# Kernel optimization log

Measured on AMD Instinct MI355X. Metric: run time of the kernel, lower is better.

Reference implementation:

```python
import jax, jax.numpy as jnp
import numpy as np

T = 1.0  # temperature from __init__


def setup_inputs() -> dict:
    key = jax.random.key(0)
    k1, k2, k3, k4, k5 = jax.random.split(key, 5)
    N, C, NC = 128, 2048, 50000
    Kp, Kn = 4, 508
    inputs = jax.random.normal(k1, (N, C), dtype=jnp.float32)
    positive_index = jax.random.randint(k2, (N, Kp), 0, NC, dtype=jnp.int64)
    negative_index = jax.random.randint(k3, (N, Kn), 0, NC, dtype=jnp.int64)
    cof = jax.random.uniform(k4, (Kp,), dtype=jnp.float32)
    # memory bank buffer (registered buffer M); L2-normalized rows like after updates
    M = jax.random.normal(k5, (NC, C), dtype=jnp.float32)
    M = M / jnp.linalg.norm(M, axis=1, keepdims=True)
    return {"inputs": inputs, "positive_index": positive_index,
            "negative_index": negative_index, "cof": cof, "M": M}


def reference(inputs, positive_index, negative_index, cof, M):
    # index_list: [N, K] with K = Kp + Kn
    index_list = jnp.concatenate([positive_index, negative_index], axis=1)
    # fused gather + batched matmul: logits[n, k] = inputs[n] . M[index_list[n, k]]
    Mg = M[index_list]                                   # [N, K, C] gather
    logits = jnp.einsum('nc,nkc->nk', inputs, Mg) * T    # [N, K]
    # the Python loop over j reuses identical logits; only the CE target column varies
    logp = jax.nn.log_softmax(logits, axis=1)            # [N, K]
    Kp = positive_index.shape[1]
    # loss = sum_j cof[j] * cross_entropy(logits, target=j) = -sum_j cof[j]*mean_n logp[n, j]
    loss = -jnp.sum(cof * jnp.mean(logp[:, :Kp], axis=0))
    return loss, logits
```

## Files before the change

### kernel.cpp

```cpp
#include <hip/hip_runtime.h>

constexpr int N  = 128;
constexpr int C  = 2048;
constexpr int KP = 4;
constexpr int KN = 508;
constexpr int K  = 512;

__global__ __launch_bounds__(256) void logits_kernel(
    const float* __restrict__ inputs,
    const int*   __restrict__ pos_idx,
    const int*   __restrict__ neg_idx,
    const float* __restrict__ M,
    float*       __restrict__ logits)
{
    const int wave = threadIdx.x >> 6;
    const int lane = threadIdx.x & 63;
    const int n    = blockIdx.y;
    const int k    = (blockIdx.x << 2) + wave;

    const int idx = (k < KP) ? pos_idx[n * KP + k]
                             : neg_idx[n * KN + (k - KP)];

    const float4* __restrict__ a = reinterpret_cast<const float4*>(inputs + (size_t)n * C);
    const float4* __restrict__ b = reinterpret_cast<const float4*>(M + (size_t)idx * C);

    float acc = 0.f;
    #pragma unroll
    for (int i = 0; i < C / (4 * 64); ++i) {
        float4 av = a[i * 64 + lane];
        float4 bv = b[i * 64 + lane];
        acc = fmaf(av.x, bv.x, acc);
        acc = fmaf(av.y, bv.y, acc);
        acc = fmaf(av.z, bv.z, acc);
        acc = fmaf(av.w, bv.w, acc);
    }

    #pragma unroll
    for (int off = 32; off > 0; off >>= 1)
        acc += __shfl_down(acc, off, 64);

    if (lane == 0) logits[n * K + k] = acc;
}

__global__ __launch_bounds__(512) void softmax_loss_kernel(
    const float* __restrict__ logits,
    const float* __restrict__ cof,
    float*       __restrict__ row_loss)
{
    __shared__ float red[8];
    __shared__ float xs[KP];
    const int n    = blockIdx.x;
    const int t    = threadIdx.x;
    const int wid  = t >> 6;
    const int lane = t & 63;

    float x = logits[n * K + t];

    float m = x;
    #pragma unroll
    for (int off = 1; off < 64; off <<= 1)
        m = fmaxf(m, __shfl_xor(m, off, 64));
    if (lane == 0) red[wid] = m;
    __syncthreads();
    float bm = red[0];
    #pragma unroll
    for (int i = 1; i < 8; ++i) bm = fmaxf(bm, red[i]);

    float s = expf(x - bm);
    #pragma unroll
    for (int off = 1; off < 64; off <<= 1)
        s += __shfl_xor(s, off, 64);
    __syncthreads();
    if (lane == 0) red[wid] = s;
    if (t < KP) xs[t] = x;
    __syncthreads();

    if (t == 0) {
        float bs = 0.f;
        #pragma unroll
        for (int i = 0; i < 8; ++i) bs += red[i];
        const float logZ = bm + logf(bs);
        float acc = 0.f;
        #pragma unroll
        for (int j = 0; j < KP; ++j)
            acc += cof[j] * (xs[j] - logZ);
        row_loss[n] = acc;
    }
}

__global__ __launch_bounds__(128) void loss_reduce_kernel(
    const float* __restrict__ row_loss,
    float*       __restrict__ out)
{
    const int t = threadIdx.x;
    float v = row_loss[t];
    #pragma unroll
    for (int off = 1; off < 64; off <<= 1)
        v += __shfl_xor(v, off, 64);
    __shared__ float red[2];
    if ((t & 63) == 0) red[t >> 6] = v;
    __syncthreads();
    if (t == 0) out[0] = -(red[0] + red[1]) / (float)N;
}

extern "C" void kernel_launch(void* const* d_in, const int* in_sizes, int n_in,
                              void* d_out, int out_size, void* d_ws, size_t ws_size,
                              hipStream_t stream) {
    const float* inputs  = (const float*)d_in[0];
    const int*   pos_idx = (const int*)d_in[1];
    const int*   neg_idx = (const int*)d_in[2];
    const float* cof     = (const float*)d_in[3];
    const float* M       = (const float*)d_in[4];

    float* out      = (float*)d_out;
    float* logits   = out + 1;
    float* row_loss = (float*)d_ws;

    logits_kernel<<<dim3(K / 4, N), 256, 0, stream>>>(inputs, pos_idx, neg_idx, M, logits);
    softmax_loss_kernel<<<N, K, 0, stream>>>(logits, cof, row_loss);
    loss_reduce_kernel<<<1, N, 0, stream>>>(row_loss, out);
}
```

Measured before the change: 82.79 us.

## Bucket-sort gather indices by memory-bank row to improve locality

Adds histogram, scan and scatter kernels that counting-sort all (n,k) pairs into buckets by gathered M row index. The logits kernel then processes pairs in bucket order, so waves running near each other read nearby M rows, which should improve cache and DRAM page locality. The cost is four extra kernel launches, atomics, and scattered reads of the inputs rows and writes of the logits. With random indices over 50000 rows, each row is rarely reused, so the locality gain may be small.

```diff
diff --git a/kernel.cpp b/kernel.cpp
--- a/kernel.cpp
+++ b/kernel.cpp
@@ -5,21 +5,72 @@
 constexpr int KP = 4;
 constexpr int KN = 508;
 constexpr int K  = 512;
+constexpr int NK = N * K;
+constexpr int NB = 1024;
+constexpr int BKT_W = 49;
+
+
+__device__ __forceinline__ int gather_idx(const int* pos_idx, const int* neg_idx, int n, int k) {
+    return (k < KP) ? pos_idx[n * KP + k] : neg_idx[n * KN + (k - KP)];
+}
+
+__global__ __launch_bounds__(1024) void zero_bins_kernel(int* __restrict__ bins) {
+    bins[threadIdx.x] = 0;
+}
+
+__global__ __launch_bounds__(256) void hist_kernel(
+    const int* __restrict__ pos_idx, const int* __restrict__ neg_idx,
+    int* __restrict__ bins)
+{
+    const int t = blockIdx.x * 256 + threadIdx.x;
+    const int n = t >> 9, k = t & (K - 1);
+    const int idx = gather_idx(pos_idx, neg_idx, n, k);
+    atomicAdd(&bins[idx / BKT_W], 1);
+}
+
+__global__ __launch_bounds__(1024) void scan_kernel(
+    const int* __restrict__ bins, int* __restrict__ offs)
+{
+    __shared__ int s[NB];
+    const int t = threadIdx.x;
+    s[t] = bins[t];
+    __syncthreads();
+    #pragma unroll
+    for (int d = 1; d < NB; d <<= 1) {
+        int v = (t >= d) ? s[t - d] : 0;
+        __syncthreads();
+        s[t] += v;
+        __syncthreads();
+    }
+    offs[t] = (t == 0) ? 0 : s[t - 1];
+}
+
+__global__ __launch_bounds__(256) void scatter_kernel(
+    const int* __restrict__ pos_idx, const int* __restrict__ neg_idx,
+    int* __restrict__ offs, int* __restrict__ sorted)
+{
+    const int t = blockIdx.x * 256 + threadIdx.x;
+    const int n = t >> 9, k = t & (K - 1);
+    const int idx = gather_idx(pos_idx, neg_idx, n, k);
+    const int p = atomicAdd(&offs[idx / BKT_W], 1);
+    sorted[p] = (n << 9) | k;
+}
 
 __global__ __launch_bounds__(256) void logits_kernel(
     const float* __restrict__ inputs,
     const int*   __restrict__ pos_idx,
     const int*   __restrict__ neg_idx,
     const float* __restrict__ M,
+    const int*   __restrict__ sorted,
     float*       __restrict__ logits)
 {
     const int wave = threadIdx.x >> 6;
     const int lane = threadIdx.x & 63;
-    const int n    = blockIdx.y;
-    const int k    = (blockIdx.x << 2) + wave;
+    const int pos  = blockIdx.x * 4 + wave;
 
-    const int idx = (k < KP) ? pos_idx[n * KP + k]
-                             : neg_idx[n * KN + (k - KP)];
+    const int packed = sorted[pos];
+    const int n = packed >> 9, k = packed & (K - 1);
+    const int idx = gather_idx(pos_idx, neg_idx, n, k);
 
     const float4* __restrict__ a = reinterpret_cast<const float4*>(inputs + (size_t)n * C);
     const float4* __restrict__ b = reinterpret_cast<const float4*>(M + (size_t)idx * C);
@@ -112,11 +163,19 @@
     const float* cof     = (const float*)d_in[3];
     const float* M       = (const float*)d_in[4];
 
-    float* out      = (float*)d_out;
-    float* logits   = out + 1;
-    float* row_loss = (float*)d_ws;
+    float* out    = (float*)d_out;
+    float* logits = out + 1;
 
-    logits_kernel<<<dim3(K / 4, N), 256, 0, stream>>>(inputs, pos_idx, neg_idx, M, logits);
+    int*   bins     = (int*)d_ws;
+    int*   offs     = bins + NB;
+    int*   sorted   = offs + NB;
+    float* row_loss = (float*)(sorted + NK);
+
+    zero_bins_kernel<<<1, NB, 0, stream>>>(bins);
+    hist_kernel<<<NK / 256, 256, 0, stream>>>(pos_idx, neg_idx, bins);
+    scan_kernel<<<1, NB, 0, stream>>>(bins, offs);
+    scatter_kernel<<<NK / 256, 256, 0, stream>>>(pos_idx, neg_idx, offs, sorted);
+    logits_kernel<<<NK / 4, 256, 0, stream>>>(inputs, pos_idx, neg_idx, M, sorted, logits);
     softmax_loss_kernel<<<N, K, 0, stream>>>(logits, cof, row_loss);
     loss_reduce_kernel<<<1, N, 0, stream>>>(row_loss, out);
 }
```

Measured after the change: 118.5 us. 43.1% more time.

## Deduplicate memory-bank row gathers via per-row bucket lists before GEMV

Applied to the files above, without the earlier changes.

Builds a per-memory-bank-row list of (n,k) requests with atomics, then launches one wave per bank row that loads the row once into registers and computes dot products for every request referencing it. This is meant to cut duplicate reads of M rows from the gather. It adds a zero pass, an atomic build pass, and many mostly-empty waves across all 50000 rows, plus an overflow path for rows requested more than 16 times. It only runs if the workspace is large enough; otherwise it falls back to the old kernel.

```diff
diff --git a/kernel.cpp b/kernel.cpp
--- a/kernel.cpp
+++ b/kernel.cpp
@@ -1,10 +1,99 @@
 #include <hip/hip_runtime.h>
 
-constexpr int N  = 128;
-constexpr int C  = 2048;
-constexpr int KP = 4;
-constexpr int KN = 508;
-constexpr int K  = 512;
+constexpr int N    = 128;
+constexpr int C    = 2048;
+constexpr int KP   = 4;
+constexpr int KN   = 508;
+constexpr int K    = 512;
+constexpr int NK   = N * K;
+constexpr int NC   = 50000;
+constexpr int MAXD = 16;
+constexpr int OCAP = 512;
+
+
+__device__ __forceinline__ int gather_idx(const int* pos_idx, const int* neg_idx, int n, int k) {
+    return (k < KP) ? pos_idx[n * KP + k] : neg_idx[n * KN + (k - KP)];
+}
+
+__global__ __launch_bounds__(256) void zero_kernel(int* __restrict__ count, int* __restrict__ ocount) {
+    const int t = blockIdx.x * 256 + threadIdx.x;
+    if (t < NC) count[t] = 0;
+    if (t == 0) *ocount = 0;
+}
+
+__global__ __launch_bounds__(256) void build_kernel(
+    const int* __restrict__ pos_idx, const int* __restrict__ neg_idx,
+    int* __restrict__ count, int* __restrict__ pairs,
+    int* __restrict__ ocount, int* __restrict__ overflow)
+{
+    const int t = blockIdx.x * 256 + threadIdx.x;
+    const int n = t >> 9, k = t & (K - 1);
+    const int idx = gather_idx(pos_idx, neg_idx, n, k);
+    const int packed = (n << 9) | k;
+    const int p = atomicAdd(&count[idx], 1);
+    if (p < MAXD) {
+        pairs[idx * MAXD + p] = packed;
+    } else {
+        const int o = atomicAdd(ocount, 1);
+        if (o < OCAP) overflow[o] = (idx << 16) | packed;
+    }
+}
+
+__global__ __launch_bounds__(256) void gemv_dedup_kernel(
+    const float* __restrict__ inputs,
+    const float* __restrict__ M,
+    const int*   __restrict__ count,
+    const int*   __restrict__ pairs,
+    const int*   __restrict__ ocount,
+    const int*   __restrict__ overflow,
+    float*       __restrict__ logits)
+{
+    const int wave = threadIdx.x >> 6;
+    const int lane = threadIdx.x & 63;
+    const int idx  = blockIdx.x * 4 + wave;
+    if (idx >= NC) return;
+
+    const int cnt = count[idx];
+    if (cnt == 0) return;
+
+    const float4* __restrict__ b = reinterpret_cast<const float4*>(M + (size_t)idx * C);
+    float4 mrow[8];
+    #pragma unroll
+    for (int i = 0; i < 8; ++i) mrow[i] = b[i * 64 + lane];
+
+    const float4* __restrict__ A = reinterpret_cast<const float4*>(inputs);
+
+    auto dot_and_store = [&](int packed) {
+        const int n = packed >> 9, k = packed & (K - 1);
+        const float4* __restrict__ a = A + (size_t)n * (C / 4);
+        float acc = 0.f;
+        #pragma unroll
+        for (int i = 0; i < 8; ++i) {
+            float4 av = a[i * 64 + lane];
+            float4 bv = mrow[i];
+            acc = fmaf(av.x, bv.x, acc);
+            acc = fmaf(av.y, bv.y, acc);
+            acc = fmaf(av.z, bv.z, acc);
+            acc = fmaf(av.w, bv.w, acc);
+        }
+        #pragma unroll
+        for (int off = 32; off > 0; off >>= 1)
+            acc += __shfl_down(acc, off, 64);
+        if (lane == 0) logits[n * K + k] = acc;
+    };
+
+    const int lim = cnt < MAXD ? cnt : MAXD;
+    for (int j = 0; j < lim; ++j)
+        dot_and_store(pairs[idx * MAXD + j]);
+
+    if (cnt > MAXD) {
+        const int oc = min(*ocount, OCAP);
+        for (int i = 0; i < oc; ++i) {
+            const int e = overflow[i];
+            if ((e >> 16) == idx) dot_and_store(e & 0xFFFF);
+        }
+    }
+}
 
 __global__ __launch_bounds__(256) void logits_kernel(
     const float* __restrict__ inputs,
@@ -34,11 +123,9 @@
         acc = fmaf(av.z, bv.z, acc);
         acc = fmaf(av.w, bv.w, acc);
     }
-
     #pragma unroll
     for (int off = 32; off > 0; off >>= 1)
         acc += __shfl_down(acc, off, 64);
-
     if (lane == 0) logits[n * K + k] = acc;
 }
 
@@ -112,11 +199,26 @@
     const float* cof     = (const float*)d_in[3];
     const float* M       = (const float*)d_in[4];
 
-    float* out      = (float*)d_out;
-    float* logits   = out + 1;
-    float* row_loss = (float*)d_ws;
-
-    logits_kernel<<<dim3(K / 4, N), 256, 0, stream>>>(inputs, pos_idx, neg_idx, M, logits);
-    softmax_loss_kernel<<<N, K, 0, stream>>>(logits, cof, row_loss);
-    loss_reduce_kernel<<<1, N, 0, stream>>>(row_loss, out);
-}
+    float* out    = (float*)d_out;
+    float* logits = out + 1;
+
+    const size_t need = (size_t)(NC + NC * MAXD + 1 + OCAP + N) * 4;
+    if (ws_size >= need) {
+        int*   count    = (int*)d_ws;
+        int*   pairs    = count + NC;
+        int*   ocount   = pairs + (size_t)NC * MAXD;
+        int*   overflow = ocount + 1;
+        float* row_loss = (float*)(overflow + OCAP);
+
+        zero_kernel<<<(NC + 255) / 256, 256, 0, stream>>>(count, ocount);
+        build_kernel<<<NK / 256, 256, 0, stream>>>(pos_idx, neg_idx, count, pairs, ocount, overflow);
+        gemv_dedup_kernel<<<(NC + 3) / 4, 256, 0, stream>>>(inputs, M, count, pairs, ocount, overflow, logits);
+        softmax_loss_kernel<<<N, K, 0, stream>>>(logits, cof, row_loss);
+        loss_reduce_kernel<<<1, N, 0, stream>>>(row_loss, out);
+    } else {
+        float* row_loss = (float*)d_ws;
+        logits_kernel<<<dim3(K / 4, N), 256, 0, stream>>>(inputs, pos_idx, neg_idx, M, logits);
+        softmax_loss_kernel<<<N, K, 0, stream>>>(logits, cof, row_loss);
+        loss_reduce_kernel<<<1, N, 0, stream>>>(row_loss, out);
+    }
+}
```

Result: no change. 83.98 us (+1.4%).
